# Optimization experiments

Hardware: AMD Instinct MI355X
Metric: run time of the kernel (lower is better)

Reference implementation:

```python
import jax, jax.numpy as jnp
import numpy as np

B, N = 1, 768
C_S, C_Z, C_H, H, P_QK, P_V = 384, 128, 16, 12, 4, 8
INF = 100000.0
EPS = 1e-8


def _points(s, w, b, rot, trans, P):
    # PointProjection: linear -> [B,N,H,3,P] -> [B,N,H,P,3] local points,
    # then global = R @ p_local + t (rigid broadcast over heads/points).
    pl = (s @ w + b).reshape(s.shape[0], s.shape[1], H, 3, P)
    pl = jnp.moveaxis(pl, -2, -1)  # [B,N,H,P,3]
    return jnp.einsum('bnij,bnhpj->bnhpi', rot, pl) + trans[:, :, None, None, :]


def setup_inputs():
    key = jax.random.key(0)
    ks = jax.random.split(key, 14)

    def lin(k, fi, fo):
        k1, k2 = jax.random.split(k)
        w = jax.random.normal(k1, (fi, fo), jnp.float32) / np.float32(np.sqrt(fi))
        b = jax.random.normal(k2, (fo,), jnp.float32) * 0.01
        return w, b

    s = jax.random.normal(ks[0], (B, N, C_S), jnp.float32)
    z = jax.random.normal(ks[1], (B, N, N, C_Z), jnp.float32)
    rot = jnp.linalg.qr(jax.random.normal(ks[2], (B, N, 3, 3), jnp.float32))[0]
    trans = jax.random.normal(ks[3], (B, N, 3), jnp.float32)
    mask = jnp.ones((B, N), jnp.float32)

    w_q, b_q = lin(ks[4], C_S, H * C_H)
    w_k, b_k = lin(ks[5], C_S, H * C_H)
    w_v, b_v = lin(ks[6], C_S, H * C_H)
    w_qp, b_qp = lin(ks[7], C_S, H * 3 * P_QK)
    w_kp, b_kp = lin(ks[8], C_S, H * 3 * P_QK)
    w_vp, b_vp = lin(ks[9], C_S, H * 3 * P_V)
    w_b, b_b = lin(ks[10], C_Z, H)
    head_weights = jax.random.normal(ks[11], (H,), jnp.float32) * 0.1
    w_o, b_o = lin(ks[12], H * (C_Z + C_H + 4 * P_V), C_S)

    return dict(s=s, z=z, rot=rot, trans=trans, mask=mask,
                w_q=w_q, b_q=b_q, w_k=w_k, b_k=b_k, w_v=w_v, b_v=b_v,
                w_qp=w_qp, b_qp=b_qp, w_kp=w_kp, b_kp=b_kp, w_vp=w_vp, b_vp=b_vp,
                w_b=w_b, b_b=b_b, head_weights=head_weights, w_o=w_o, b_o=b_o)


def reference(s, z, rot, trans, mask,
              w_q, b_q, w_k, b_k, w_v, b_v,
              w_qp, b_qp, w_kp, b_kp, w_vp, b_vp,
              w_b, b_b, head_weights, w_o, b_o):
    # per-head point weights: sqrt(2 / (9 * P_QK)) * softplus(head_weights)
    pw = np.float32(np.sqrt(2.0 / (9.0 * P_QK))) * jnp.logaddexp(head_weights, 0.0)  # [H]

    q_pts = _points(s, w_qp, b_qp, rot, trans, P_QK)  # [B,N,H,P,3]
    k_pts = _points(s, w_kp, b_kp, rot, trans, P_QK)

    # sum_p ||q_p - k_p||^2 expanded: |q|^2 + |k|^2 - 2 q.k (summed over p,xyz)
    qk_pt = jnp.einsum('bqhpc,bkhpc->bqkh', q_pts, k_pts)
    q2 = jnp.sum(q_pts * q_pts, axis=(-2, -1))  # [B,N,H]
    k2 = jnp.sum(k_pts * k_pts, axis=(-2, -1))
    pt_att = -0.5 * pw * (q2[:, :, None, :] + k2[:, None, :, :] - 2.0 * qk_pt)  # [B,Nq,Nk,H]

    q = (s @ w_q + b_q).reshape(B, N, H, C_H) * np.float32(np.sqrt(1.0 / C_H))
    k = (s @ w_k + b_k).reshape(B, N, H, C_H)
    a = pt_att + jnp.einsum('bqhc,bkhc->bqkh', q, k)
    a = a + (z @ w_b + b_b)  # pair bias [B,Nq,Nk,H]

    sq_mask = mask[:, :, None] * mask[:, None, :]
    a = a + (INF * (sq_mask - 1.0))[..., None]
    a = jax.nn.softmax(a * np.float32(np.sqrt(1.0 / 3.0)), axis=-2)  # softmax over k

    v = (s @ w_v + b_v).reshape(B, N, H, C_H)
    o = jnp.einsum('bqkh,bkhc->bqhc', a, v).reshape(B, N, H * C_H)

    v_pts = _points(s, w_vp, b_vp, rot, trans, P_V)  # [B,N,H,P,3]
    o_pt = jnp.einsum('bqkh,bkhpc->bqhpc', a, v_pts).reshape(B, N, H * P_V, 3)
    # inverse rigid: R^T @ (p - t)
    o_pt = jnp.einsum('bnji,bnpj->bnpi', rot, o_pt - trans[:, :, None, :])  # [B,N,H*P_V,3]
    o_pt_norm = jnp.sqrt(jnp.sum(o_pt * o_pt, axis=-1) + EPS)  # [B,N,H*P_V]

    o_pair = jnp.einsum('bqkh,bqkc->bqhc', a, z).reshape(B, N, H * C_Z)

    cat = jnp.concatenate(
        [o, o_pt[..., 0], o_pt[..., 1], o_pt[..., 2], o_pt_norm, o_pair], axis=-1)
    return cat @ w_o + b_o  # [B,N,C_S]
```

## Files before the change

kernel.cpp:

```cpp
#include <hip/hip_runtime.h>
#include <math.h>

#define NN 768
#define KALL 1152
#define CATD 2112
#define INF_ 100000.0f
#define PACKN (385 * KALL)

__device__ __forceinline__ float4 ld4(const float* p) { return *(const float4*)p; }

__device__ __forceinline__ float qsum_dpp(float v) {
  v += __int_as_float(__builtin_amdgcn_mov_dpp(__float_as_int(v), 0xB1, 0xF, 0xF, true));
  v += __int_as_float(__builtin_amdgcn_mov_dpp(__float_as_int(v), 0x4E, 0xF, 0xF, true));
  return v;
}

__global__ __launch_bounds__(256) void pack_kernel(
    const float* wq, const float* bq, const float* wk, const float* bk,
    const float* wv, const float* bv, const float* wqp, const float* bqp,
    const float* wkp, const float* bkp, const float* wvp, const float* bvp,
    const float* wbm, float* Wall, float* ball, float* wtr) {
  int idx = blockIdx.x * 256 + threadIdx.x;
  if (idx >= PACKN + 1536) return;
  if (idx >= PACKN) {
    int u = idx - PACKN;
    int h = u >> 7, c = u & 127;
    wtr[u] = wbm[c * 12 + h];
    return;
  }
  int kk = idx / KALL, u = idx - kk * KALL;
  const float *w, *b; int col, dim; float sc = 1.f;
  if (u < 192)      { w = wq;  b = bq;  col = u;       dim = 192; sc = 0.25f; }
  else if (u < 384) { w = wk;  b = bk;  col = u - 192; dim = 192; }
  else if (u < 576) { w = wv;  b = bv;  col = u - 384; dim = 192; }
  else if (u < 720) { w = wqp; b = bqp; col = u - 576; dim = 144; }
  else if (u < 864) { w = wkp; b = bkp; col = u - 720; dim = 144; }
  else              { w = wvp; b = bvp; col = u - 864; dim = 288; }
  if (kk < 384) Wall[kk * KALL + u] = sc * w[kk * dim + col];
  else          ball[u] = sc * b[col];
}

__global__ __launch_bounds__(256) void proj_kernel(const float* s, const float* Wall,
                                                   const float* ball, float* proj) {
  int q0 = blockIdx.x * 32, c0 = blockIdx.y * 64;
  int tid = threadIdx.x;
  int qa = q0 + (tid >> 4) * 2, qb = qa + 1;
  int c = c0 + (tid & 15) * 4;
  const float* sa = s + qa * 384;
  const float* sb = s + qb * 384;
  const float* wp = Wall + c;
  float4 acc0 = {0, 0, 0, 0}, acc1 = {0, 0, 0, 0};
#pragma unroll 4
  for (int k = 0; k < 384; k++) {
    float4 w4 = ld4(wp + k * KALL);
    float a0 = sa[k], a1 = sb[k];
    acc0.x += a0 * w4.x; acc0.y += a0 * w4.y; acc0.z += a0 * w4.z; acc0.w += a0 * w4.w;
    acc1.x += a1 * w4.x; acc1.y += a1 * w4.y; acc1.z += a1 * w4.z; acc1.w += a1 * w4.w;
  }
  float4 b4 = ld4(ball + c);
  acc0.x += b4.x; acc0.y += b4.y; acc0.z += b4.z; acc0.w += b4.w;
  acc1.x += b4.x; acc1.y += b4.y; acc1.z += b4.z; acc1.w += b4.w;
  *(float4*)(proj + (size_t)qa * KALL + c) = acc0;
  *(float4*)(proj + (size_t)qb * KALL + c) = acc1;
}

__global__ __launch_bounds__(256) void points_kernel(const float* proj, const float* rot,
                                                     const float* trans, float* qpts, float* kpts,
                                                     float* vpts, float* q2, float* k2) {
  int n = blockIdx.x, tid = threadIdx.x;
  __shared__ float sq[12], sk[12];
  if (tid < 12) { sq[tid] = 0.f; sk[tid] = 0.f; }
  __syncthreads();
  if (tid < 192) {
    const float* R = rot + n * 9;
    const float* T = trans + n * 3;
    const float* pr = proj + (size_t)n * KALL;
    int base, P; float* outp; int h; bool isq = false, isk = false;
    if (tid < 48)      { h = tid >> 2; int p = tid & 3; base = 576 + h * 12; P = 4;
                         outp = qpts + n * 144 + h * 12 + p * 3; base += p; isq = true; }
    else if (tid < 96) { int i = tid - 48; h = i >> 2; int p = i & 3; base = 720 + h * 12; P = 4;
                         outp = kpts + n * 144 + h * 12 + p * 3; base += p; isk = true; }
    else               { int i = tid - 96; h = i >> 3; int p = i & 7; base = 864 + h * 24; P = 8;
                         outp = vpts + n * 288 + h * 24 + p * 3; base += p; }
    float l0 = pr[base], l1 = pr[base + P], l2 = pr[base + 2 * P];
    float g0 = R[0] * l0 + R[1] * l1 + R[2] * l2 + T[0];
    float g1 = R[3] * l0 + R[4] * l1 + R[5] * l2 + T[1];
    float g2 = R[6] * l0 + R[7] * l1 + R[8] * l2 + T[2];
    outp[0] = g0; outp[1] = g1; outp[2] = g2;
    float ns = g0 * g0 + g1 * g1 + g2 * g2;
    if (isq) atomicAdd(&sq[h], ns);
    else if (isk) atomicAdd(&sk[h], ns);
  }
  __syncthreads();
  if (tid < 12) { q2[n * 12 + tid] = sq[tid]; k2[n * 12 + tid] = sk[tid]; }
}

__global__ __launch_bounds__(256, 4) void bias_kernel(const float* __restrict__ z,
                                                      const float* __restrict__ wtr,
                                                      const float* __restrict__ bb,
                                                      float* __restrict__ abuf) {
  int q = blockIdx.x, k0 = blockIdx.y * 96;
  int tid = threadIdx.x;
  int lane = tid & 63;
  int wv = tid >> 6;
  int grp = lane >> 5;
  int cl = lane & 31;
  __shared__ float lsm[96 * 100];

  float4 w4[12];
#pragma unroll
  for (int h = 0; h < 12; h++) w4[h] = ld4(wtr + h * 128 + cl * 4);

  const float* zq = z + ((size_t)q * NN + k0) * 128;
  int rbase = wv * 24;
  int quad = cl >> 2, sub = cl & 3;
#pragma unroll 2
  for (int it = 0; it < 12; it++) {
    int rloc = rbase + it * 2 + grp;
    float4 z4 = ld4(zq + (size_t)rloc * 128 + cl * 4);
    float a[12];
#pragma unroll
    for (int h = 0; h < 12; h++)
      a[h] = z4.x * w4[h].x + z4.y * w4[h].y + z4.z * w4[h].z + z4.w * w4[h].w;
#pragma unroll
    for (int h = 0; h < 12; h++) a[h] = qsum_dpp(a[h]);
    bool s1 = (sub == 1), s2 = (sub == 2);
    float vx = s1 ? a[4] : (s2 ? a[8]  : a[0]);
    float vy = s1 ? a[5] : (s2 ? a[9]  : a[1]);
    float vz = s1 ? a[6] : (s2 ? a[10] : a[2]);
    float vw = s1 ? a[7] : (s2 ? a[11] : a[3]);
    if (sub < 3) {
      float* p = lsm + rloc * 100 + quad * 12 + sub * 4;
      *(float4*)p = make_float4(vx, vy, vz, vw);
    }
  }
  __syncthreads();
  for (int i = tid; i < 96 * 12; i += 256) {
    int h = i / 96, k = i - h * 96;
    const float* p = lsm + k * 100 + h;
    float ssum = bb[h];
#pragma unroll
    for (int g = 0; g < 8; g++) ssum += p[g * 12];
    abuf[((size_t)q * 12 + h) * NN + k0 + k] = ssum;
  }
}

__global__ __launch_bounds__(256) void softmax_kernel(const float* proj, const float* qpts,
                                                      const float* kpts, const float* q2,
                                                      const float* k2, const float* mask,
                                                      const float* hw, float* abuf) {
  int q0 = blockIdx.x * 8, h = blockIdx.y;
  int tid = threadIdx.x;
  __shared__ float qw[8][16], qp[8][12], q2s[8], mq[8], red[4][8], row[8], pws;
  if (tid < 128) qw[tid >> 4][tid & 15] = proj[(size_t)(q0 + (tid >> 4)) * KALL + h * 16 + (tid & 15)];
  else if (tid < 224) { int i = tid - 128; qp[i / 12][i % 12] = qpts[(q0 + i / 12) * 144 + h * 12 + i % 12]; }
  else if (tid < 232) q2s[tid - 224] = q2[(q0 + tid - 224) * 12 + h];
  else if (tid < 240) mq[tid - 232] = mask[q0 + tid - 232];
  else if (tid == 240) {
    float x = hw[h];
    pws = 0.23570226039551584f * (fmaxf(x, 0.f) + log1pf(__expf(-fabsf(x))));
  }
  __syncthreads();

  float L[3][8];
#pragma unroll
  for (int i = 0; i < 3; i++) {
    int kk = i * 256 + tid;
    float kw[16], kp[12];
    const float* kwp = proj + (size_t)kk * KALL + 192 + h * 16;
    *(float4*)(kw) = ld4(kwp); *(float4*)(kw + 4) = ld4(kwp + 4);
    *(float4*)(kw + 8) = ld4(kwp + 8); *(float4*)(kw + 12) = ld4(kwp + 12);
    const float* kpp = kpts + (size_t)kk * 144 + h * 12;
    *(float4*)(kp) = ld4(kpp); *(float4*)(kp + 4) = ld4(kpp + 4); *(float4*)(kp + 8) = ld4(kpp + 8);
    float k2v = k2[kk * 12 + h];
    float mk = mask[kk];
#pragma unroll
    for (int q = 0; q < 8; q++) {
      float4 qa = *(const float4*)&qw[q][0];
      float4 qb = *(const float4*)&qw[q][4];
      float4 qc = *(const float4*)&qw[q][8];
      float4 qd = *(const float4*)&qw[q][12];
      float4 pa = *(const float4*)&qp[q][0];
      float4 pb = *(const float4*)&qp[q][4];
      float4 pc = *(const float4*)&qp[q][8];
      float d = qa.x * kw[0] + qa.y * kw[1] + qa.z * kw[2] + qa.w * kw[3]
              + qb.x * kw[4] + qb.y * kw[5] + qb.z * kw[6] + qb.w * kw[7]
              + qc.x * kw[8] + qc.y * kw[9] + qc.z * kw[10] + qc.w * kw[11]
              + qd.x * kw[12] + qd.y * kw[13] + qd.z * kw[14] + qd.w * kw[15];
      float dp = pa.x * kp[0] + pa.y * kp[1] + pa.z * kp[2] + pa.w * kp[3]
               + pb.x * kp[4] + pb.y * kp[5] + pb.z * kp[6] + pb.w * kp[7]
               + pc.x * kp[8] + pc.y * kp[9] + pc.z * kp[10] + pc.w * kp[11];
      float bias = abuf[((size_t)(q0 + q) * 12 + h) * NN + kk];
      float val = bias + d - 0.5f * pws * (q2s[q] + k2v - 2.f * dp) + INF_ * (mq[q] * mk - 1.f);
      L[i][q] = val * 0.5773502691896258f;
    }
  }
  float m[8];
#pragma unroll
  for (int q = 0; q < 8; q++) m[q] = fmaxf(fmaxf(L[0][q], L[1][q]), L[2][q]);
#pragma unroll
  for (int d = 1; d < 64; d <<= 1)
#pragma unroll
    for (int q = 0; q < 8; q++) m[q] = fmaxf(m[q], __shfl_xor(m[q], d, 64));
  int wv = tid >> 6;
  if ((tid & 63) == 0)
    for (int q = 0; q < 8; q++) red[wv][q] = m[q];
  __syncthreads();
  if (tid < 8) row[tid] = fmaxf(fmaxf(red[0][tid], red[1][tid]), fmaxf(red[2][tid], red[3][tid]));
  __syncthreads();
  float sm[8];
#pragma unroll
  for (int q = 0; q < 8; q++) {
    float mm = row[q];
    L[0][q] = __expf(L[0][q] - mm);
    L[1][q] = __expf(L[1][q] - mm);
    L[2][q] = __expf(L[2][q] - mm);
    sm[q] = L[0][q] + L[1][q] + L[2][q];
  }
#pragma unroll
  for (int d = 1; d < 64; d <<= 1)
#pragma unroll
    for (int q = 0; q < 8; q++) sm[q] += __shfl_xor(sm[q], d, 64);
  if ((tid & 63) == 0)
    for (int q = 0; q < 8; q++) red[wv][q] = sm[q];
  __syncthreads();
  if (tid < 8) row[tid] = 1.f / (red[0][tid] + red[1][tid] + red[2][tid] + red[3][tid]);
  __syncthreads();
#pragma unroll
  for (int q = 0; q < 8; q++) {
    float r = row[q];
    float* ap = abuf + ((size_t)(q0 + q) * 12 + h) * NN + tid;
    ap[0] = L[0][q] * r; ap[256] = L[1][q] * r; ap[512] = L[2][q] * r;
  }
}

__global__ __launch_bounds__(256) void opair_kernel(const float* __restrict__ z,
                                                    const float* __restrict__ abuf,
                                                    float* __restrict__ cat) {
  int q = blockIdx.x, tid = threadIdx.x;
  int cq = tid & 31;
  int g  = tid >> 5;
  __shared__ float red[8 * 1540];
  const float* zp = z + ((size_t)q * NN + g * 96) * 128 + cq * 4;
  const float* ap = abuf + (size_t)q * 12 * NN + g * 96;
  float acc[12][4];
#pragma unroll
  for (int h = 0; h < 12; h++) { acc[h][0] = 0.f; acc[h][1] = 0.f; acc[h][2] = 0.f; acc[h][3] = 0.f; }
  for (int r = 0; r < 96; r += 4) {
    float4 z0 = ld4(zp + (size_t)(r + 0) * 128);
    float4 z1 = ld4(zp + (size_t)(r + 1) * 128);
    float4 z2 = ld4(zp + (size_t)(r + 2) * 128);
    float4 z3 = ld4(zp + (size_t)(r + 3) * 128);
#pragma unroll
    for (int h = 0; h < 12; h++) {
      float4 a4 = ld4(ap + h * NN + r);
      acc[h][0] += a4.x * z0.x + a4.y * z1.x + a4.z * z2.x + a4.w * z3.x;
      acc[h][1] += a4.x * z0.y + a4.y * z1.y + a4.z * z2.y + a4.w * z3.y;
      acc[h][2] += a4.x * z0.z + a4.y * z1.z + a4.z * z2.z + a4.w * z3.z;
      acc[h][3] += a4.x * z0.w + a4.y * z1.w + a4.z * z2.w + a4.w * z3.w;
    }
  }
#pragma unroll
  for (int h = 0; h < 12; h++)
    *(float4*)(red + g * 1540 + h * 128 + cq * 4) = *(float4*)acc[h];
  __syncthreads();
#pragma unroll
  for (int i = 0; i < 6; i++) {
    int idx = i * 256 + tid;
    float ssum = 0.f;
#pragma unroll
    for (int gg = 0; gg < 8; gg++) ssum += red[gg * 1540 + idx];
    cat[(size_t)q * CATD + 576 + idx] = ssum;
  }
}

__global__ __launch_bounds__(256) void ovpart_kernel(const float* proj, const float* vpts,
                                                     const float* abuf, float* pov) {
  int h = blockIdx.x, q0 = blockIdx.y * 32, kz = blockIdx.z;
  int tid = threadIdx.x;
  int qg = tid >> 3, jb = tid & 7;
  int q = q0 + qg;
  const float* ap = abuf + ((size_t)q * 12 + h) * NN + kz * 192;
  const float* vp = proj + (size_t)(kz * 192) * KALL + 384 + h * 16;
  const float* vpp = vpts + (size_t)(kz * 192) * 288 + h * 24;
  float acc[5] = {0, 0, 0, 0, 0};
  for (int k = 0; k < 192; k += 4) {
    float4 a4 = ld4(ap + k);
    const float af[4] = {a4.x, a4.y, a4.z, a4.w};
#pragma unroll
    for (int kk = 0; kk < 4; kk++) {
      float av = af[kk];
      size_t kr = k + kk;
      acc[0] += av * vp[kr * KALL + jb];
      acc[1] += av * vp[kr * KALL + jb + 8];
      acc[2] += av * vpp[kr * 288 + jb];
      acc[3] += av * vpp[kr * 288 + jb + 8];
      acc[4] += av * vpp[kr * 288 + jb + 16];
    }
  }
  float* o = pov + (((size_t)kz * 768 + q) * 12 + h) * 40;
  o[jb] = acc[0]; o[jb + 8] = acc[1];
  o[16 + jb] = acc[2]; o[16 + jb + 8] = acc[3]; o[16 + jb + 16] = acc[4];
}

__global__ __launch_bounds__(256) void ovred_kernel(const float* pov, const float* rot,
                                                    const float* trans, float* cat) {
  int q = blockIdx.x, tid = threadIdx.x;
  const float* pq = pov + (size_t)q * 480;
  if (tid < 96) {
    int h = tid >> 3, p = tid & 7;
    float x = 0.f, y = 0.f, zz = 0.f;
#pragma unroll
    for (int j = 0; j < 4; j++) {
      const float* b = pq + (size_t)j * 768 * 480 + h * 40 + 16 + p * 3;
      x += b[0]; y += b[1]; zz += b[2];
    }
    const float* R = rot + q * 9;
    const float* T = trans + q * 3;
    float dx = x - T[0], dy = y - T[1], dz = zz - T[2];
    float lx = R[0] * dx + R[3] * dy + R[6] * dz;
    float ly = R[1] * dx + R[4] * dy + R[7] * dz;
    float lz = R[2] * dx + R[5] * dy + R[8] * dz;
    float nrm = sqrtf(lx * lx + ly * ly + lz * lz + 1e-8f);
    int hp = h * 8 + p;
    float* co = cat + (size_t)q * CATD;
    co[192 + hp] = lx; co[288 + hp] = ly; co[384 + hp] = lz; co[480 + hp] = nrm;
  } else {
    int i = tid - 96;
    int h = i >> 4, c = i & 15;
    float s = 0.f;
#pragma unroll
    for (int j = 0; j < 4; j++) s += pq[(size_t)j * 768 * 480 + h * 40 + c];
    cat[(size_t)q * CATD + h * 16 + c] = s;
    if (i < 32) {
      int i2 = i + 160;
      int h2 = i2 >> 4, c2 = i2 & 15;
      float s2 = 0.f;
#pragma unroll
      for (int j = 0; j < 4; j++) s2 += pq[(size_t)j * 768 * 480 + h2 * 40 + c2];
      cat[(size_t)q * CATD + h2 * 16 + c2] = s2;
    }
  }
}

__global__ __launch_bounds__(256) void out_part_kernel(const float* cat, const float* wo,
                                                       float* part) {
  int q0 = blockIdx.x * 16, c0 = blockIdx.y * 64, k0 = blockIdx.z * 264;
  int tid = threadIdx.x;
  int q = q0 + (tid >> 4);
  int c = c0 + (tid & 15) * 4;
  const float* cp = cat + (size_t)q * CATD + k0;
  const float* wp = wo + (size_t)k0 * 384 + c;
  float4 acc = {0, 0, 0, 0};
#pragma unroll 8
  for (int k = 0; k < 264; k++) {
    float a = cp[k];
    float4 w4 = ld4(wp + (size_t)k * 384);
    acc.x += a * w4.x; acc.y += a * w4.y; acc.z += a * w4.z; acc.w += a * w4.w;
  }
  *(float4*)(part + ((size_t)blockIdx.z * 768 + q) * 384 + c) = acc;
}

__global__ __launch_bounds__(256) void out_reduce_kernel(const float* part, const float* bo,
                                                         float* out) {
  int idx = blockIdx.x * 256 + threadIdx.x;
  int q = idx / 96, cg = idx - q * 96;
  int c = cg * 4;
  float4 acc = ld4(bo + c);
#pragma unroll
  for (int j = 0; j < 8; j++) {
    float4 p = ld4(part + ((size_t)j * 768 + q) * 384 + c);
    acc.x += p.x; acc.y += p.y; acc.z += p.z; acc.w += p.w;
  }
  *(float4*)(out + (size_t)q * 384 + c) = acc;
}

extern "C" void kernel_launch(void* const* d_in, const int* in_sizes, int n_in,
                              void* d_out, int out_size, void* d_ws, size_t ws_size,
                              hipStream_t stream) {
  const float* s     = (const float*)d_in[0];
  const float* z     = (const float*)d_in[1];
  const float* rot   = (const float*)d_in[2];
  const float* trans = (const float*)d_in[3];
  const float* mask  = (const float*)d_in[4];
  const float* wq    = (const float*)d_in[5];
  const float* bq    = (const float*)d_in[6];
  const float* wk    = (const float*)d_in[7];
  const float* bk    = (const float*)d_in[8];
  const float* wv    = (const float*)d_in[9];
  const float* bv    = (const float*)d_in[10];
  const float* wqp   = (const float*)d_in[11];
  const float* bqp   = (const float*)d_in[12];
  const float* wkp   = (const float*)d_in[13];
  const float* bkp   = (const float*)d_in[14];
  const float* wvp   = (const float*)d_in[15];
  const float* bvp   = (const float*)d_in[16];
  const float* wb    = (const float*)d_in[17];
  const float* bb    = (const float*)d_in[18];
  const float* hw    = (const float*)d_in[19];
  const float* wo    = (const float*)d_in[20];
  const float* bo    = (const float*)d_in[21];
  float* out = (float*)d_out;

  float* ws = (float*)d_ws;
  float* proj  = ws;
  float* Wall  = proj + 884736;
  float* ball  = Wall + 442368;
  float* qpts  = ball + 1152;
  float* kpts  = qpts + 110592;
  float* vpts  = kpts + 110592;
  float* q2    = vpts + 221184;
  float* k2    = q2 + 9216;
  float* abuf  = k2 + 9216;
  float* cat   = abuf + 7077888;
  float* part  = cat + 1622016;
  float* wtr   = part + 2359296;
  float* pov   = wtr + 2048;

  pack_kernel<<<dim3((PACKN + 1536 + 255) / 256), 256, 0, stream>>>(
      wq, bq, wk, bk, wv, bv, wqp, bqp, wkp, bkp, wvp, bvp, wb, Wall, ball, wtr);
  proj_kernel<<<dim3(24, 18), 256, 0, stream>>>(s, Wall, ball, proj);
  points_kernel<<<dim3(768), 256, 0, stream>>>(proj, rot, trans, qpts, kpts, vpts, q2, k2);
  bias_kernel<<<dim3(768, 8), 256, 0, stream>>>(z, wtr, bb, abuf);
  softmax_kernel<<<dim3(96, 12), 256, 0, stream>>>(proj, qpts, kpts, q2, k2, mask, hw, abuf);
  opair_kernel<<<dim3(768), 256, 0, stream>>>(z, abuf, cat);
  ovpart_kernel<<<dim3(12, 24, 4), 256, 0, stream>>>(proj, vpts, abuf, pov);
  ovred_kernel<<<dim3(768), 256, 0, stream>>>(pov, rot, trans, cat);
  out_part_kernel<<<dim3(48, 6, 8), 256, 0, stream>>>(cat, wo, part);
  out_reduce_kernel<<<dim3(288), 256, 0, stream>>>(part, bo, out);
}
```

Baseline: 766.0 us.

## Pack per-head key and value data into contiguous head-major buffers

The points kernel now writes per-head packed buffers: keys (16 k features, 12 point coords, k2 norm, mask, padded to 32) and values (16 v features plus 24 point coords, 40 per row), laid out head-major. Softmax and ovpart then read contiguous rows instead of strided gathers from the wide projection buffer and separate point arrays. The projection kernel is also changed to one query row per thread with twice as many blocks. This costs an extra pass writing the packed buffers and gives up the reuse of each weight load across two rows in the projection kernel.

```diff
diff --git a/kernel.cpp b/kernel.cpp
--- a/kernel.cpp
+++ b/kernel.cpp
@@ -42,34 +42,32 @@
 
 __global__ __launch_bounds__(256) void proj_kernel(const float* s, const float* Wall,
                                                    const float* ball, float* proj) {
-  int q0 = blockIdx.x * 32, c0 = blockIdx.y * 64;
   int tid = threadIdx.x;
-  int qa = q0 + (tid >> 4) * 2, qb = qa + 1;
-  int c = c0 + (tid & 15) * 4;
-  const float* sa = s + qa * 384;
-  const float* sb = s + qb * 384;
+  int q = blockIdx.x * 16 + (tid >> 4);
+  int c = blockIdx.y * 64 + (tid & 15) * 4;
+  const float* sa = s + q * 384;
   const float* wp = Wall + c;
-  float4 acc0 = {0, 0, 0, 0}, acc1 = {0, 0, 0, 0};
+  float4 acc = {0, 0, 0, 0};
 #pragma unroll 4
   for (int k = 0; k < 384; k++) {
     float4 w4 = ld4(wp + k * KALL);
-    float a0 = sa[k], a1 = sb[k];
-    acc0.x += a0 * w4.x; acc0.y += a0 * w4.y; acc0.z += a0 * w4.z; acc0.w += a0 * w4.w;
-    acc1.x += a1 * w4.x; acc1.y += a1 * w4.y; acc1.z += a1 * w4.z; acc1.w += a1 * w4.w;
+    float a0 = sa[k];
+    acc.x += a0 * w4.x; acc.y += a0 * w4.y; acc.z += a0 * w4.z; acc.w += a0 * w4.w;
   }
   float4 b4 = ld4(ball + c);
-  acc0.x += b4.x; acc0.y += b4.y; acc0.z += b4.z; acc0.w += b4.w;
-  acc1.x += b4.x; acc1.y += b4.y; acc1.z += b4.z; acc1.w += b4.w;
-  *(float4*)(proj + (size_t)qa * KALL + c) = acc0;
-  *(float4*)(proj + (size_t)qb * KALL + c) = acc1;
+  acc.x += b4.x; acc.y += b4.y; acc.z += b4.z; acc.w += b4.w;
+  *(float4*)(proj + (size_t)q * KALL + c) = acc;
 }
 
 __global__ __launch_bounds__(256) void points_kernel(const float* proj, const float* rot,
-                                                     const float* trans, float* qpts, float* kpts,
-                                                     float* vpts, float* q2, float* k2) {
+                                                     const float* trans, const float* mask,
+                                                     float* qpts, float* q2,
+                                                     float* kpack, float* vpack) {
   int n = blockIdx.x, tid = threadIdx.x;
-  __shared__ float sq[12], sk[12];
+  __shared__ float sq[12], sk[12], kp_s[144], vp_s[288];
+  __shared__ float mk_s;
   if (tid < 12) { sq[tid] = 0.f; sk[tid] = 0.f; }
+  if (tid == 12) mk_s = mask[n];
   __syncthreads();
   if (tid < 192) {
     const float* R = rot + n * 9;
@@ -79,9 +77,9 @@
     if (tid < 48)      { h = tid >> 2; int p = tid & 3; base = 576 + h * 12; P = 4;
                          outp = qpts + n * 144 + h * 12 + p * 3; base += p; isq = true; }
     else if (tid < 96) { int i = tid - 48; h = i >> 2; int p = i & 3; base = 720 + h * 12; P = 4;
-                         outp = kpts + n * 144 + h * 12 + p * 3; base += p; isk = true; }
+                         outp = kp_s + h * 12 + p * 3; base += p; isk = true; }
     else               { int i = tid - 96; h = i >> 3; int p = i & 7; base = 864 + h * 24; P = 8;
-                         outp = vpts + n * 288 + h * 24 + p * 3; base += p; }
+                         outp = vp_s + h * 24 + p * 3; base += p; }
     float l0 = pr[base], l1 = pr[base + P], l2 = pr[base + 2 * P];
     float g0 = R[0] * l0 + R[1] * l1 + R[2] * l2 + T[0];
     float g1 = R[3] * l0 + R[4] * l1 + R[5] * l2 + T[1];
@@ -92,7 +90,23 @@
     else if (isk) atomicAdd(&sk[h], ns);
   }
   __syncthreads();
-  if (tid < 12) { q2[n * 12 + tid] = sq[tid]; k2[n * 12 + tid] = sk[tid]; }
+  const float* prn = proj + (size_t)n * KALL;
+  for (int i = tid; i < 384; i += 256) {
+    int h = i >> 5, j = i & 31;
+    float v;
+    if (j < 16)      v = prn[192 + h * 16 + j];
+    else if (j < 28) v = kp_s[h * 12 + (j - 16)];
+    else if (j == 28) v = sk[h];
+    else if (j == 29) v = mk_s;
+    else             v = 0.f;
+    kpack[((size_t)h * NN + n) * 32 + j] = v;
+  }
+  for (int i = tid; i < 480; i += 256) {
+    int h = i / 40, j = i - h * 40;
+    float v = (j < 16) ? prn[384 + h * 16 + j] : vp_s[h * 24 + (j - 16)];
+    vpack[((size_t)h * NN + n) * 40 + j] = v;
+  }
+  if (tid < 12) q2[n * 12 + tid] = sq[tid];
 }
 
 __global__ __launch_bounds__(256, 4) void bias_kernel(const float* __restrict__ z,
@@ -146,9 +160,10 @@
 }
 
 __global__ __launch_bounds__(256) void softmax_kernel(const float* proj, const float* qpts,
-                                                      const float* kpts, const float* q2,
-                                                      const float* k2, const float* mask,
-                                                      const float* hw, float* abuf) {
+                                                      const float* q2, const float* mask,
+                                                      const float* hw,
+                                                      const float* __restrict__ kpack,
+                                                      float* abuf) {
   int q0 = blockIdx.x * 8, h = blockIdx.y;
   int tid = threadIdx.x;
   __shared__ float qw[8][16], qp[8][12], q2s[8], mq[8], red[4][8], row[8], pws;
@@ -167,13 +182,13 @@
   for (int i = 0; i < 3; i++) {
     int kk = i * 256 + tid;
     float kw[16], kp[12];
-    const float* kwp = proj + (size_t)kk * KALL + 192 + h * 16;
-    *(float4*)(kw) = ld4(kwp); *(float4*)(kw + 4) = ld4(kwp + 4);
-    *(float4*)(kw + 8) = ld4(kwp + 8); *(float4*)(kw + 12) = ld4(kwp + 12);
-    const float* kpp = kpts + (size_t)kk * 144 + h * 12;
-    *(float4*)(kp) = ld4(kpp); *(float4*)(kp + 4) = ld4(kpp + 4); *(float4*)(kp + 8) = ld4(kpp + 8);
-    float k2v = k2[kk * 12 + h];
-    float mk = mask[kk];
+    const float* kpp = kpack + ((size_t)h * NN + kk) * 32;
+    *(float4*)(kw) = ld4(kpp); *(float4*)(kw + 4) = ld4(kpp + 4);
+    *(float4*)(kw + 8) = ld4(kpp + 8); *(float4*)(kw + 12) = ld4(kpp + 12);
+    *(float4*)(kp) = ld4(kpp + 16); *(float4*)(kp + 4) = ld4(kpp + 20); *(float4*)(kp + 8) = ld4(kpp + 24);
+    float4 t4 = ld4(kpp + 28);
+    float k2v = t4.x;
+    float mk = t4.y;
 #pragma unroll
     for (int q = 0; q < 8; q++) {
       float4 qa = *(const float4*)&qw[q][0];
@@ -274,15 +289,15 @@
   }
 }
 
-__global__ __launch_bounds__(256) void ovpart_kernel(const float* proj, const float* vpts,
-                                                     const float* abuf, float* pov) {
+__global__ __launch_bounds__(256) void ovpart_kernel(const float* __restrict__ vpack,
+                                                     const float* __restrict__ abuf,
+                                                     float* pov) {
   int h = blockIdx.x, q0 = blockIdx.y * 32, kz = blockIdx.z;
   int tid = threadIdx.x;
   int qg = tid >> 3, jb = tid & 7;
   int q = q0 + qg;
   const float* ap = abuf + ((size_t)q * 12 + h) * NN + kz * 192;
-  const float* vp = proj + (size_t)(kz * 192) * KALL + 384 + h * 16;
-  const float* vpp = vpts + (size_t)(kz * 192) * 288 + h * 24;
+  const float* vk = vpack + ((size_t)h * NN + kz * 192) * 40;
   float acc[5] = {0, 0, 0, 0, 0};
   for (int k = 0; k < 192; k += 4) {
     float4 a4 = ld4(ap + k);
@@ -290,12 +305,12 @@
 #pragma unroll
     for (int kk = 0; kk < 4; kk++) {
       float av = af[kk];
-      size_t kr = k + kk;
-      acc[0] += av * vp[kr * KALL + jb];
-      acc[1] += av * vp[kr * KALL + jb + 8];
-      acc[2] += av * vpp[kr * 288 + jb];
-      acc[3] += av * vpp[kr * 288 + jb + 8];
-      acc[4] += av * vpp[kr * 288 + jb + 16];
+      const float* vr = vk + (size_t)(k + kk) * 40;
+      acc[0] += av * vr[jb];
+      acc[1] += av * vr[jb + 8];
+      acc[2] += av * vr[16 + jb];
+      acc[3] += av * vr[24 + jb];
+      acc[4] += av * vr[32 + jb];
     }
   }
   float* o = pov + (((size_t)kz * 768 + q) * 12 + h) * 40;
@@ -407,24 +422,23 @@
   float* Wall  = proj + 884736;
   float* ball  = Wall + 442368;
   float* qpts  = ball + 1152;
-  float* kpts  = qpts + 110592;
-  float* vpts  = kpts + 110592;
-  float* q2    = vpts + 221184;
-  float* k2    = q2 + 9216;
-  float* abuf  = k2 + 9216;
+  float* q2    = qpts + 110592;
+  float* kpack = q2 + 9216;
+  float* vpack = kpack + 294912;
+  float* abuf  = vpack + 368640;
   float* cat   = abuf + 7077888;
   float* part  = cat + 1622016;
   float* wtr   = part + 2359296;
-  float* pov   = wtr + 2048;
+  float* pov   = wtr + 1536;
 
   pack_kernel<<<dim3((PACKN + 1536 + 255) / 256), 256, 0, stream>>>(
       wq, bq, wk, bk, wv, bv, wqp, bqp, wkp, bkp, wvp, bvp, wb, Wall, ball, wtr);
-  proj_kernel<<<dim3(24, 18), 256, 0, stream>>>(s, Wall, ball, proj);
-  points_kernel<<<dim3(768), 256, 0, stream>>>(proj, rot, trans, qpts, kpts, vpts, q2, k2);
+  proj_kernel<<<dim3(48, 18), 256, 0, stream>>>(s, Wall, ball, proj);
+  points_kernel<<<dim3(768), 256, 0, stream>>>(proj, rot, trans, mask, qpts, q2, kpack, vpack);
   bias_kernel<<<dim3(768, 8), 256, 0, stream>>>(z, wtr, bb, abuf);
-  softmax_kernel<<<dim3(96, 12), 256, 0, stream>>>(proj, qpts, kpts, q2, k2, mask, hw, abuf);
+  softmax_kernel<<<dim3(96, 12), 256, 0, stream>>>(proj, qpts, q2, mask, hw, kpack, abuf);
   opair_kernel<<<dim3(768), 256, 0, stream>>>(z, abuf, cat);
-  ovpart_kernel<<<dim3(12, 24, 4), 256, 0, stream>>>(proj, vpts, abuf, pov);
+  ovpart_kernel<<<dim3(12, 24, 4), 256, 0, stream>>>(vpack, abuf, pov);
   ovred_kernel<<<dim3(768), 256, 0, stream>>>(pov, rot, trans, cat);
   out_part_kernel<<<dim3(48, 6, 8), 256, 0, stream>>>(cat, wo, part);
   out_reduce_kernel<<<dim3(288), 256, 0, stream>>>(part, bo, out);
```

New measurement: 780.6 us. About the same (+1.9%).
